# Kernel optimization log

Measured on AMD Instinct MI355X. Metric: run time of the kernel, lower is better.

## Reference

```python
import jax, jax.numpy as jnp
import numpy as np

B, INP, OUP = 16, 64, 64
T, H, W = 30, 64, 44
KD, KH, KW = 3, 3, 3
M, G = 2, 2
INP_GAP = max(16, INP // 16)          # 16
GROUPS = G * OUP                       # 128 (wn_fc2 groups)
IN_PG = (M * OUP) // GROUPS            # 1  in-channels per group
OUT_PG = (OUP * INP * KD * KH * KW) // GROUPS  # 864 out-channels per group


def setup_inputs() -> dict:
    key = jax.random.key(0)
    ks = jax.random.split(key, 6)
    x = jax.random.normal(ks[0], (B, INP, T, H, W), dtype=jnp.float32)
    # reduce: 1x1x1 conv INP -> INP_GAP (with bias), acts on [B, INP, 1,1,1]
    w_reduce = jax.random.normal(ks[1], (INP_GAP, INP), dtype=jnp.float32) * 0.05
    b_reduce = jax.random.normal(ks[2], (INP_GAP,), dtype=jnp.float32) * 0.05
    # wn_fc1: 1x1x1 conv INP_GAP -> M*OUP (with bias)
    w_fc1 = jax.random.normal(ks[3], (M * OUP, INP_GAP), dtype=jnp.float32) * 0.05
    b_fc1 = jax.random.normal(ks[4], (M * OUP,), dtype=jnp.float32) * 0.05
    # wn_fc2: grouped 1x1x1 conv, no bias: [groups, out_per_group, in_per_group]
    w_fc2 = jax.random.normal(ks[5], (GROUPS, OUT_PG, IN_PG), dtype=jnp.float32) * 0.02
    return {"x": x, "w_reduce": w_reduce, "b_reduce": b_reduce,
            "w_fc1": w_fc1, "b_fc1": b_fc1, "w_fc2": w_fc2}


def reference(x, w_reduce, b_reduce, w_fc1, b_fc1, w_fc2):
    # Global average pool over T,H,W -> [B, INP]; 1x1x1 convs are matmuls.
    x_gap = x.mean(axis=(2, 3, 4))                       # [B, INP]
    g = x_gap @ w_reduce.T + b_reduce                     # [B, INP_GAP]
    h = jax.nn.sigmoid(g @ w_fc1.T + b_fc1)               # [B, M*OUP]
    # Grouped 1x1 conv (groups=GROUPS): group-major channel layout matches
    # torch's conv output ordering, so a plain reshape reproduces .view().
    hg = h.reshape(B, GROUPS, IN_PG)                      # [B, G*OUP, 1]
    wdyn = jnp.einsum('goi,bgi->bgo', w_fc2, hg)          # [B, GROUPS, OUT_PG]
    wdyn = wdyn.reshape(B, OUP, INP, KD, KH, KW)          # per-sample conv weights

    # Per-sample conv3d (groups=1), stride 1, padding 1 on D,H,W.
    def conv_one(xi, wi):
        # xi: [INP, T, H, W], wi: [OUP, INP, KD, KH, KW]
        return jax.lax.conv_general_dilated(
            xi[None], wi, window_strides=(1, 1, 1),
            padding=[(1, 1), (1, 1), (1, 1)],
            dimension_numbers=('NCDHW', 'OIDHW', 'NCDHW'))[0]

    return jax.vmap(conv_one)(x, wdyn)                    # [B, OUP, T, H, W]
```

## Files before the change

### kernel.cpp

```cpp
#include <hip/hip_runtime.h>
#include <hip/hip_bf16.h>
#include <stdint.h>

#define B_ 16
#define T_ 30
#define H_ 64
#define W_ 44
#define HW_ (H_*W_)
#define THW_ (T_*HW_)

#define HP_ 66
#define WP_ 46
#define PPLANE_ (HP_*WP_)
#define PPOS_ (T_*PPLANE_)

#define NS3 576

#define SWZ(v) (((v) >> 1) & 3)

typedef __bf16 bf16x8 __attribute__((ext_vector_type(8)));
typedef float f32x4 __attribute__((ext_vector_type(4)));

static __device__ __forceinline__ short f2bf(float f) {
    __hip_bfloat16 h = __float2bfloat16(f);
    union { __hip_bfloat16 b; short s; } u; u.b = h; return u.s;
}

static __device__ __forceinline__ void gload_lds16(const short* g, short* l) {
    __builtin_amdgcn_global_load_lds((const __attribute__((address_space(1))) void*)g,
                                     (__attribute__((address_space(3))) void*)l, 16, 0, 0);
}

__global__ __launch_bounds__(256) void transpose_kernel(const float* __restrict__ x,
                                                        short* __restrict__ xt,
                                                        float* __restrict__ gap) {
    __shared__ short lb[64*52];
    __shared__ float gsum[64];
    int blk = blockIdx.x;
    int b = blk / (T_*HP_);
    int r = blk - b*(T_*HP_);
    int t = r / HP_;
    int hp = r - t*HP_;
    int tid = threadIdx.x;
    bool interior = (hp >= 1) && (hp <= H_);
    float rsum = 0.f;
    {
        int ic = tid >> 2, g = tid & 3;
        if (interior) {
            int h = hp - 1;
            const float4* row = (const float4*)(x + ((size_t)(b*64 + ic)*T_ + t)*HW_ + h*W_);
            #pragma unroll
            for (int q = g; q < 11; q += 4) {
                float4 v = row[q];
                short4 s4;
                s4.x = f2bf(v.x); s4.y = f2bf(v.y); s4.z = f2bf(v.z); s4.w = f2bf(v.w);
                *(short4*)&lb[ic*52 + q*4] = s4;
                rsum += (v.x + v.y) + (v.z + v.w);
            }
        }
        rsum += __shfl_xor(rsum, 1);
        rsum += __shfl_xor(rsum, 2);
        if ((tid & 3) == 0) gsum[ic] = rsum;
    }
    __syncthreads();
    if (interior && tid < 64)
        atomicAdd(&gap[b*64 + tid], gsum[tid] * (1.0f / THW_));
    for (int e = tid; e < WP_*16; e += 256) {
        int wp = e >> 4, i4 = (e & 15) * 4;
        short4 s4 = make_short4(0,0,0,0);
        if (interior && wp >= 1 && wp <= W_) {
            int w = wp - 1;
            s4.x = lb[(i4+0)*52 + w];
            s4.y = lb[(i4+1)*52 + w];
            s4.z = lb[(i4+2)*52 + w];
            s4.w = lb[(i4+3)*52 + w];
        }
        size_t pos = (size_t)t*PPLANE_ + hp*WP_ + wp;
        short* dst = xt + ((size_t)(b*2 + (i4 >> 5))*PPOS_ + pos)*32 + (i4 & 31);
        *(short4*)dst = s4;
    }
}

__global__ __launch_bounds__(256) void fc_kernel(const float* __restrict__ gap,
        const float* __restrict__ w_reduce, const float* __restrict__ b_reduce,
        const float* __restrict__ w_fc1, const float* __restrict__ b_fc1,
        float* __restrict__ h_out) {
    __shared__ float gl[256];
    int t = threadIdx.x;
    {
        int b = t >> 4, j = t & 15;
        float a = b_reduce[j];
        #pragma unroll
        for (int c = 0; c < 64; ++c) a += gap[b*64 + c] * w_reduce[j*64 + c];
        gl[b*16 + j] = a;
    }
    __syncthreads();
    for (int idx = t; idx < 2048; idx += 256) {
        int b = idx >> 7, j = idx & 127;
        float v = b_fc1[j];
        #pragma unroll
        for (int i = 0; i < 16; ++i) v += gl[b*16 + i] * w_fc1[j*16 + i];
        h_out[idx] = 1.0f / (1.0f + expf(-v));
    }
}

__global__ __launch_bounds__(256) void wdyn_kernel(const float* __restrict__ w_fc2,
        const float* __restrict__ h, short* __restrict__ wdyn, short* __restrict__ zblk) {
    if (blockIdx.x == 0 && threadIdx.x < 128) zblk[threadIdx.x] = 0;
    int b = blockIdx.x / 27, tap = blockIdx.x % 27;
    short* dst = wdyn + ((size_t)b*27 + tap) * 4096;
    for (int e = threadIdx.x; e < 4096; e += 256) {
        int oc = e >> 6, ic = e & 63;
        float wv = w_fc2[(oc*64 + ic)*27 + tap];
        float hv = h[b*128 + 2*oc + (ic >> 5)];
        dst[e] = f2bf(wv * hv);
    }
}

#define MF4(J, BV) do {                                                \
    acc[0][J] = __builtin_amdgcn_mfma_f32_16x16x32_bf16(a0, BV, acc[0][J], 0, 0, 0); \
    acc[1][J] = __builtin_amdgcn_mfma_f32_16x16x32_bf16(a1, BV, acc[1][J], 0, 0, 0); \
    acc[2][J] = __builtin_amdgcn_mfma_f32_16x16x32_bf16(a2, BV, acc[2][J], 0, 0, 0); \
    acc[3][J] = __builtin_amdgcn_mfma_f32_16x16x32_bf16(a3, BV, acc[3][J], 0, 0, 0); \
} while (0)

#define DO_TAP(tap, bank) do {                                         \
    int _kd = (tap)/9, _rm = (tap)-9*_kd, _kh = _rm/3, _kw = _rm-3*_kh;\
    int _sb = (tzw + _kd)*144 + (hw + _kh)*18 + _kw + ln;              \
    bf16x8 b0_, b1_, b2_, a0, a1, a2, a3;                              \
    b0_ = *(const bf16x8*)&xs[(_sb    )*32 + ((kg ^ SWZ(_sb    ))*8)]; \
    b1_ = *(const bf16x8*)&xs[(_sb+18)*32 + ((kg ^ SWZ(_sb+18))*8)];   \
    b2_ = *(const bf16x8*)&xs[(_sb+36)*32 + ((kg ^ SWZ(_sb+36))*8)];   \
    {                                                                  \
        const short* _wq = &wb[0][0] + (bank)*2048;                    \
        int _cw = (kg ^ SWZ(ln)) * 8;                                  \
        a0 = *(const bf16x8*)&_wq[(ln     )*32 + _cw];                 \
        a1 = *(const bf16x8*)&_wq[(ln + 16)*32 + _cw];                 \
        a2 = *(const bf16x8*)&_wq[(ln + 32)*32 + _cw];                 \
        a3 = *(const bf16x8*)&_wq[(ln + 48)*32 + _cw];                 \
    }                                                                  \
    __builtin_amdgcn_s_setprio(1);                                     \
    MF4(0, b0_); MF4(1, b1_); MF4(2, b2_);                             \
    __builtin_amdgcn_s_setprio(0);                                     \
} while (0)

__global__ __launch_bounds__(256, 3) void conv_kernel(const short* __restrict__ xt,
        const short* __restrict__ wdyn, const short* __restrict__ zblk,
        float* __restrict__ out) {
    __shared__ short xs[NS3*32];
    __shared__ short wb[2][2048];

    int bid = (blockIdx.x & 7) * 990 + (blockIdx.x >> 3);
    int b = bid / 495; int r = bid - b*495;
    int tzt = r / 33; r -= tzt*33;
    int tyt = r / 3;  int txt = r - tyt*3;
    int t0 = tzt*2, h0 = tyt*6, w0 = txt*16;

    int tid = threadIdx.x, wid = tid >> 6, lane = tid & 63;
    int ln = lane & 15, kg = lane >> 4;
    int l4 = lane >> 2, c = lane & 3;
    int tzw = wid & 1, hw = (wid >> 1) * 3;
    int woc = tid >> 2, wseg = tid & 3;

    const short* wdb   = wdyn + (size_t)b * 27 * 4096;
    const short* wbase = wdb + woc*64 + wseg*8;
    short* wdst0 = &wb[0][0] + woc*32 + ((wseg ^ SWZ(woc)) * 8);
    short* wdst1 = wdst0 + 2048;

    f32x4 acc[4][3];
    #pragma unroll
    for (int mt = 0; mt < 4; ++mt)
        #pragma unroll
        for (int j = 0; j < 3; ++j) acc[mt][j] = f32x4{0.f, 0.f, 0.f, 0.f};

    auto wload = [&](int gn) {
        int tap = gn - ((gn >= 27) ? 27 : 0);
        int nh  = (gn >= 27) ? 32 : 0;
        return *(const uint4*)(wbase + tap*4096 + nh);
    };
    auto stage_x = [&](int half) {
        const short* xbh = xt + (size_t)(b*2 + half) * PPOS_ * 32;
        #pragma unroll
        for (int ii = 0; ii < 9; ++ii) {
            int inst = ii*4 + wid;
            int s = inst*16 + l4;
            int z = s / 144; int rr = s - z*144;
            int y = rr / 18; int xx = rr - y*18;
            int t = t0 + z - 1;
            int hp = h0 + y;
            int seg = (c ^ SWZ(s)) * 8;
            const short* src = ((unsigned)t < (unsigned)T_ && hp < HP_)
                ? xbh + ((size_t)t*PPLANE_ + hp*WP_ + (w0+xx))*32 + seg
                : zblk + seg;
            gload_lds16(src, xs + inst*512);
        }
    };

    stage_x(0);
    uint4 wr0 = wload(0), wr1 = wload(1);
    asm volatile("s_waitcnt vmcnt(0)" ::: "memory");
    __builtin_amdgcn_s_barrier();

    #pragma unroll 1
    for (int rd = 0; rd < 13; ++rd) {
        int g0 = 2*rd;
        __syncthreads();
        *(uint4*)wdst0 = wr0;
        *(uint4*)wdst1 = wr1;
        __syncthreads();
        wr0 = wload(g0 + 2);
        wr1 = wload(g0 + 3);
        DO_TAP(g0,     0);
        DO_TAP(g0 + 1, 1);
    }
    __syncthreads();
    *(uint4*)wdst0 = wr0;
    __syncthreads();
    wr0 = wload(28);
    DO_TAP(26, 0);
    __syncthreads();
    stage_x(1);
    asm volatile("s_waitcnt vmcnt(0)" ::: "memory");
    __builtin_amdgcn_s_barrier();
    *(uint4*)wdst1 = wr1;
    __syncthreads();
    wr1 = wload(29);
    DO_TAP(0, 1);
    #pragma unroll 1
    for (int rd = 0; rd < 13; ++rd) {
        int g0 = 28 + 2*rd;
        __syncthreads();
        *(uint4*)wdst0 = wr0;
        *(uint4*)wdst1 = wr1;
        __syncthreads();
        if (rd < 12) { wr0 = wload(g0 + 2); wr1 = wload(g0 + 3); }
        DO_TAP(g0 - 27, 0);
        DO_TAP(g0 - 26, 1);
    }

    int t = t0 + tzw;
    int wv = w0 + ln;
    if (wv < W_) {
        #pragma unroll
        for (int mt = 0; mt < 4; ++mt) {
            size_t obase = ((size_t)(b*64 + mt*16 + kg*4) * T_ + t) * HW_;
            #pragma unroll
            for (int j = 0; j < 3; ++j) {
                int hh = h0 + hw + j;
                if (hh < H_) {
                    float* o = out + obase + hh*W_ + wv;
                    #pragma unroll
                    for (int ri = 0; ri < 4; ++ri)
                        o[(size_t)ri * THW_] = acc[mt][j][ri];
                }
            }
        }
    }
}

extern "C" void kernel_launch(void* const* d_in, const int* in_sizes, int n_in,
                              void* d_out, int out_size, void* d_ws, size_t ws_size,
                              hipStream_t stream) {
    const float* x        = (const float*)d_in[0];
    const float* w_reduce = (const float*)d_in[1];
    const float* b_reduce = (const float*)d_in[2];
    const float* w_fc1    = (const float*)d_in[3];
    const float* b_fc1    = (const float*)d_in[4];
    const float* w_fc2    = (const float*)d_in[5];
    float* out = (float*)d_out;

    float* gap  = (float*)d_ws;
    float* h    = gap + 1024;
    short* wdyn = (short*)(h + 2048);
    short* zblk = wdyn + (size_t)B_*27*4096;
    short* xt   = zblk + 128;

    hipMemsetAsync(gap, 0, 1024*sizeof(float), stream);
    transpose_kernel<<<B_*T_*HP_, 256, 0, stream>>>(x, xt, gap);
    fc_kernel       <<<1,         256, 0, stream>>>(gap, w_reduce, b_reduce, w_fc1, b_fc1, h);
    wdyn_kernel     <<<B_*27,     256, 0, stream>>>(w_fc2, h, wdyn, zblk);
    conv_kernel     <<<B_*495,    256, 0, stream>>>(xt, wdyn, zblk, out);
}
```

Baseline: 540.8 us.

## Software-pipeline conv tap loop with single barrier and prefetched activation fragments

Restructures the conv main loop into one 54-step loop that uses a single barrier per tap instead of two. Each step stores the next tap's weights into the alternate LDS bank and prefetches the next tap's activation fragments into registers while the MFMAs for the current tap run. The aim is to cut barrier count and hide LDS read latency behind matrix work. In exchange it needs more registers for the n0-n2 buffers, which could push against the 3-blocks occupancy bound, and it depends on subtle bank-parity synchronisation being correct.

Result: slower. 568.5 us (+5.1%).

```diff
diff --git a/kernel.cpp b/kernel.cpp
--- a/kernel.cpp
+++ b/kernel.cpp
@@ -117,6 +117,11 @@
     }
 }
 
+#define RAWBAR() do {                                                  \
+    asm volatile("s_waitcnt lgkmcnt(0)" ::: "memory");                 \
+    __builtin_amdgcn_s_barrier();                                      \
+} while (0)
+
 #define MF4(J, BV) do {                                                \
     acc[0][J] = __builtin_amdgcn_mfma_f32_16x16x32_bf16(a0, BV, acc[0][J], 0, 0, 0); \
     acc[1][J] = __builtin_amdgcn_mfma_f32_16x16x32_bf16(a1, BV, acc[1][J], 0, 0, 0); \
@@ -124,24 +129,13 @@
     acc[3][J] = __builtin_amdgcn_mfma_f32_16x16x32_bf16(a3, BV, acc[3][J], 0, 0, 0); \
 } while (0)
 
-#define DO_TAP(tap, bank) do {                                         \
-    int _kd = (tap)/9, _rm = (tap)-9*_kd, _kh = _rm/3, _kw = _rm-3*_kh;\
+#define BREADN(gn, N0, N1, N2) do {                                    \
+    int _tap = (gn) - (((gn) >= 27) ? 27 : 0);                         \
+    int _kd = _tap/9, _rm = _tap-9*_kd, _kh = _rm/3, _kw = _rm-3*_kh;  \
     int _sb = (tzw + _kd)*144 + (hw + _kh)*18 + _kw + ln;              \
-    bf16x8 b0_, b1_, b2_, a0, a1, a2, a3;                              \
-    b0_ = *(const bf16x8*)&xs[(_sb    )*32 + ((kg ^ SWZ(_sb    ))*8)]; \
-    b1_ = *(const bf16x8*)&xs[(_sb+18)*32 + ((kg ^ SWZ(_sb+18))*8)];   \
-    b2_ = *(const bf16x8*)&xs[(_sb+36)*32 + ((kg ^ SWZ(_sb+36))*8)];   \
-    {                                                                  \
-        const short* _wq = &wb[0][0] + (bank)*2048;                    \
-        int _cw = (kg ^ SWZ(ln)) * 8;                                  \
-        a0 = *(const bf16x8*)&_wq[(ln     )*32 + _cw];                 \
-        a1 = *(const bf16x8*)&_wq[(ln + 16)*32 + _cw];                 \
-        a2 = *(const bf16x8*)&_wq[(ln + 32)*32 + _cw];                 \
-        a3 = *(const bf16x8*)&_wq[(ln + 48)*32 + _cw];                 \
-    }                                                                  \
-    __builtin_amdgcn_s_setprio(1);                                     \
-    MF4(0, b0_); MF4(1, b1_); MF4(2, b2_);                             \
-    __builtin_amdgcn_s_setprio(0);                                     \
+    N0 = *(const bf16x8*)&xs[(_sb    )*32 + ((kg ^ SWZ(_sb    ))*8)];  \
+    N1 = *(const bf16x8*)&xs[(_sb+18)*32 + ((kg ^ SWZ(_sb+18))*8)];   \
+    N2 = *(const bf16x8*)&xs[(_sb+36)*32 + ((kg ^ SWZ(_sb+36))*8)];   \
 } while (0)
 
 __global__ __launch_bounds__(256, 3) void conv_kernel(const short* __restrict__ xt,
@@ -164,8 +158,7 @@
 
     const short* wdb   = wdyn + (size_t)b * 27 * 4096;
     const short* wbase = wdb + woc*64 + wseg*8;
-    short* wdst0 = &wb[0][0] + woc*32 + ((wseg ^ SWZ(woc)) * 8);
-    short* wdst1 = wdst0 + 2048;
+    short* wdst = &wb[0][0] + woc*32 + ((wseg ^ SWZ(woc)) * 8);
 
     f32x4 acc[4][3];
     #pragma unroll
@@ -197,45 +190,40 @@
     };
 
     stage_x(0);
-    uint4 wr0 = wload(0), wr1 = wload(1);
+    uint4 wr = wload(0);
     asm volatile("s_waitcnt vmcnt(0)" ::: "memory");
-    __builtin_amdgcn_s_barrier();
+    *(uint4*)wdst = wr;
+    wr = wload(1);
+    RAWBAR();
+    bf16x8 a0, a1, a2, a3, b0, b1, b2, n0, n1, n2;
+    BREADN(0, b0, b1, b2);
 
     #pragma unroll 1
-    for (int rd = 0; rd < 13; ++rd) {
-        int g0 = 2*rd;
-        __syncthreads();
-        *(uint4*)wdst0 = wr0;
-        *(uint4*)wdst1 = wr1;
-        __syncthreads();
-        wr0 = wload(g0 + 2);
-        wr1 = wload(g0 + 3);
-        DO_TAP(g0,     0);
-        DO_TAP(g0 + 1, 1);
-    }
-    __syncthreads();
-    *(uint4*)wdst0 = wr0;
-    __syncthreads();
-    wr0 = wload(28);
-    DO_TAP(26, 0);
-    __syncthreads();
-    stage_x(1);
-    asm volatile("s_waitcnt vmcnt(0)" ::: "memory");
-    __builtin_amdgcn_s_barrier();
-    *(uint4*)wdst1 = wr1;
-    __syncthreads();
-    wr1 = wload(29);
-    DO_TAP(0, 1);
-    #pragma unroll 1
-    for (int rd = 0; rd < 13; ++rd) {
-        int g0 = 28 + 2*rd;
-        __syncthreads();
-        *(uint4*)wdst0 = wr0;
-        *(uint4*)wdst1 = wr1;
-        __syncthreads();
-        if (rd < 12) { wr0 = wload(g0 + 2); wr1 = wload(g0 + 3); }
-        DO_TAP(g0 - 27, 0);
-        DO_TAP(g0 - 26, 1);
+    for (int g = 0; g < 54; ++g) {
+        RAWBAR();
+        if (g < 53)
+            *(uint4*)(wdst + (((g + 1) & 1) << 11)) = wr;
+        if (g < 52) wr = wload(g + 2);
+        {
+            const short* wq = &wb[0][0] + ((g & 1) << 11);
+            int cw = (kg ^ SWZ(ln)) * 8;
+            a0 = *(const bf16x8*)&wq[(ln     )*32 + cw];
+            a1 = *(const bf16x8*)&wq[(ln + 16)*32 + cw];
+            a2 = *(const bf16x8*)&wq[(ln + 32)*32 + cw];
+            a3 = *(const bf16x8*)&wq[(ln + 48)*32 + cw];
+        }
+        if (g < 53 && g != 26) BREADN(g + 1, n0, n1, n2);
+        __builtin_amdgcn_s_setprio(1);
+        MF4(0, b0); MF4(1, b1); MF4(2, b2);
+        __builtin_amdgcn_s_setprio(0);
+        if (g == 26) {
+            RAWBAR();
+            stage_x(1);
+            asm volatile("s_waitcnt vmcnt(0)" ::: "memory");
+            __builtin_amdgcn_s_barrier();
+            BREADN(27, n0, n1, n2);
+        }
+        b0 = n0; b1 = n1; b2 = n2;
     }
 
     int t = t0 + tzw;
```
